# Optimization experiments

Hardware: AMD Instinct MI355X
Metric: run time of the kernel (lower is better)

## Reference

```python
import jax, jax.numpy as jnp
import numpy as np

EMBED_DIM = 1024
N_TOKENS = 4096


def setup_inputs() -> dict:
    key = jax.random.key(0)
    k1, k2, k3 = jax.random.split(key, 3)
    inputs = jax.random.normal(k1, (N_TOKENS, EMBED_DIM), dtype=jnp.float32)
    rotation_params = jax.random.normal(k2, (EMBED_DIM, EMBED_DIM), dtype=jnp.float32)
    entangle_params = jax.random.normal(k3, (EMBED_DIM, EMBED_DIM), dtype=jnp.float32)
    return {"inputs": inputs, "rotation_params": rotation_params, "entangle_params": entangle_params}


def reference(inputs, rotation_params, entangle_params):
    d = EMBED_DIM
    wq = rotation_params.reshape(d, -1)
    wk = entangle_params.reshape(d, -1)
    query = inputs @ wq                      # [N, d_k]
    key = inputs @ wk                        # [N, d_k]
    scale = 1.0 / np.sqrt(d).astype(np.float32)
    scores = jax.nn.softmax((query @ key.T) * scale, axis=-1)  # [N, N]
    return scores @ inputs                   # [N, d]
```

## Files before the change

kernel.cpp:

```cpp
#include <hip/hip_runtime.h>

#define EMBED 1024
#define NTOK  4096
#define MARGIN 256.0f
#define KC     8
#define CAP    128

#define SX_INV 25.4f
#define SQ_INV 0.0155029296875f
#define SCLOGIT 0.07936198f

typedef short  s16x8 __attribute__((ext_vector_type(8)));
typedef float  f32x4 __attribute__((ext_vector_type(4)));
typedef int    i32x4 __attribute__((ext_vector_type(4)));

__device__ __forceinline__ unsigned short f2bf(float f) {
    unsigned int u = __float_as_uint(f);
    u = (u + 0x7FFFu + ((u >> 16) & 1u)) >> 16;
    return (unsigned short)u;
}
__device__ __forceinline__ float bf2f(unsigned short h) {
    return __uint_as_float(((unsigned int)h) << 16);
}

__device__ __forceinline__ void async16(const void* g, void* l) {
    __builtin_amdgcn_global_load_lds(
        (const __attribute__((address_space(1))) unsigned int*)g,
        (__attribute__((address_space(3))) unsigned int*)l, 16, 0, 0);
}

template<int ROWS>
__device__ __forceinline__ void stage_rows(const char* __restrict__ g,
                                           int ld, char* lds, int wave, int lane) {
#pragma unroll
    for (int r = 0; r < ROWS / 64; ++r) {
        const int row0 = (wave * (ROWS / 64) + r) * 16;
        const int r_loc = lane >> 2;
        const int kc = (lane - (lane >> 3)) & 3;
        const char* gp = g + (size_t)(row0 + r_loc) * ld + kc * 16;
        char* lp = lds + row0 * 64;
        async16(gp, lp);
    }
}

__device__ __forceinline__ int frag_slot(int row, int kc) {
    return (kc + ((row & 15) >> 1)) & 3;
}
__device__ __forceinline__ s16x8 frag_bf16(const char* lds, int row, int kc) {
    return *(const s16x8*)(lds + row * 64 + frag_slot(row, kc) * 16);
}
__device__ __forceinline__ i32x4 frag_i8(const char* lds, int row, int kc) {
    return *(const i32x4*)(lds + row * 64 + frag_slot(row, kc) * 16);
}

template<int BM, int BN, int SPLIT, int EPI, int NCH>
__global__ __launch_bounds__(256) void gemm_mfma(
        const unsigned short* __restrict__ Ahi, const unsigned short* __restrict__ Alo,
        const unsigned short* __restrict__ Bhi, const unsigned short* __restrict__ Blo,
        float* __restrict__ C, unsigned short* __restrict__ Chi,
        unsigned short* __restrict__ Clo, signed char* __restrict__ Ci8,
        int K, int lda, int ldb, int ldc, float scale)
{
    constexpr int TM = BM / 2, TN = BN / 2;
    constexpr int IM = TM / 16, IN = TN / 16;

    __shared__ __align__(16) char As_hi[BM * 64 * NCH];
    __shared__ __align__(16) char Bs_hi[BN * 64 * NCH];
    __shared__ __align__(16) char As_lo[SPLIT == 3 ? BM * 64 * NCH : 16];
    __shared__ __align__(16) char Bs_lo[SPLIT == 3 ? BN * 64 * NCH : 16];

    const int t = threadIdx.x;
    const int lane = t & 63, wave = t >> 6;
    const int wm = wave >> 1, wn = wave & 1;
    const int m0 = blockIdx.y * BM, n0 = blockIdx.x * BN;

    f32x4 acc[IM][IN];
#pragma unroll
    for (int i = 0; i < IM; ++i)
#pragma unroll
        for (int j = 0; j < IN; ++j)
#pragma unroll
            for (int r = 0; r < 4; ++r) acc[i][j][r] = 0.f;

    const char* ah_g = (const char*)(Ahi + (size_t)m0 * lda);
    const char* bh_g = (const char*)(Bhi + (size_t)n0 * ldb);
    const char* al_g = (SPLIT == 3) ? (const char*)(Alo + (size_t)m0 * lda) : nullptr;
    const char* bl_g = (SPLIT == 3) ? (const char*)(Blo + (size_t)n0 * ldb) : nullptr;

    const int kc = lane >> 4;
    const int rr = lane & 15;

    for (int k0 = 0; k0 < K; k0 += 32 * NCH) {
#pragma unroll
        for (int c = 0; c < NCH; ++c) {
            const int kb = (k0 + 32 * c) * 2;
            stage_rows<BM>(ah_g + kb, lda * 2, As_hi + c * BM * 64, wave, lane);
            stage_rows<BN>(bh_g + kb, ldb * 2, Bs_hi + c * BN * 64, wave, lane);
            if constexpr (SPLIT == 3) {
                stage_rows<BM>(al_g + kb, lda * 2, As_lo + c * BM * 64, wave, lane);
                stage_rows<BN>(bl_g + kb, ldb * 2, Bs_lo + c * BN * 64, wave, lane);
            }
        }
        __syncthreads();

#pragma unroll
        for (int c = 0; c < NCH; ++c) {
            s16x8 ah[IM], bh[IN], al[IM], bl[IN];
#pragma unroll
            for (int i = 0; i < IM; ++i)
                ah[i] = frag_bf16(As_hi + c * BM * 64, wm * TM + i * 16 + rr, kc);
#pragma unroll
            for (int j = 0; j < IN; ++j)
                bh[j] = frag_bf16(Bs_hi + c * BN * 64, wn * TN + j * 16 + rr, kc);
            if constexpr (SPLIT == 3) {
#pragma unroll
                for (int i = 0; i < IM; ++i)
                    al[i] = frag_bf16(As_lo + c * BM * 64, wm * TM + i * 16 + rr, kc);
#pragma unroll
                for (int j = 0; j < IN; ++j)
                    bl[j] = frag_bf16(Bs_lo + c * BN * 64, wn * TN + j * 16 + rr, kc);
            }

#pragma unroll
            for (int i = 0; i < IM; ++i)
#pragma unroll
                for (int j = 0; j < IN; ++j)
                    acc[i][j] = __builtin_amdgcn_mfma_f32_16x16x32_bf16(ah[i], bh[j], acc[i][j], 0, 0, 0);
            if constexpr (SPLIT == 3) {
#pragma unroll
                for (int i = 0; i < IM; ++i)
#pragma unroll
                    for (int j = 0; j < IN; ++j)
                        acc[i][j] = __builtin_amdgcn_mfma_f32_16x16x32_bf16(ah[i], bl[j], acc[i][j], 0, 0, 0);
#pragma unroll
                for (int i = 0; i < IM; ++i)
#pragma unroll
                    for (int j = 0; j < IN; ++j)
                        acc[i][j] = __builtin_amdgcn_mfma_f32_16x16x32_bf16(al[i], bh[j], acc[i][j], 0, 0, 0);
            }
        }
        __syncthreads();
    }

    const int lr = lane >> 4;
    const int lc = lane & 15;
#pragma unroll
    for (int i = 0; i < IM; ++i)
#pragma unroll
        for (int j = 0; j < IN; ++j)
#pragma unroll
            for (int r = 0; r < 4; ++r) {
                const int row = m0 + wm * TM + i * 16 + lr * 4 + r;
                const int col = n0 + wn * TN + j * 16 + lc;
                const float v = acc[i][j][r] * scale;
                const size_t idx = (size_t)row * ldc + col;
                if constexpr (EPI == 1) {
                    const unsigned short h = f2bf(v);
                    Chi[idx] = h;
                    Clo[idx] = f2bf(v - bf2f(h));
                } else {
                    C[idx] = v;
                    const float q = fminf(fmaxf(v * SQ_INV, -127.f), 127.f);
                    Ci8[idx] = (signed char)(int)rintf(q);
                }
            }
}

__global__ __launch_bounds__(256) void gemm_i8_scores(
        const signed char* __restrict__ A,
        const signed char* __restrict__ B,
        float* __restrict__ tmax, int* __restrict__ cnts, int2* __restrict__ cand)
{
    __shared__ __align__(16) char As[128 * 64 * 2];
    __shared__ __align__(16) char Bs[128 * 64 * 2];

    const int t = threadIdx.x;
    const int lane = t & 63, wave = t >> 6;
    const int wm = wave >> 1, wn = wave & 1;
    const int m0 = blockIdx.y * 128, n0 = blockIdx.x * 128;

    i32x4 acc[4][4];
#pragma unroll
    for (int i = 0; i < 4; ++i)
#pragma unroll
        for (int j = 0; j < 4; ++j)
#pragma unroll
            for (int r = 0; r < 4; ++r) acc[i][j][r] = 0;

    const char* a_g = (const char*)A + (size_t)m0 * EMBED;
    const char* b_g = (const char*)B + (size_t)n0 * EMBED;
    const int kc = lane >> 4;
    const int rr = lane & 15;

    for (int k0 = 0; k0 < EMBED; k0 += 128) {
#pragma unroll
        for (int c = 0; c < 2; ++c) {
            stage_rows<128>(a_g + k0 + 64 * c, EMBED, As + c * 128 * 64, wave, lane);
            stage_rows<128>(b_g + k0 + 64 * c, EMBED, Bs + c * 128 * 64, wave, lane);
        }
        __syncthreads();

#pragma unroll
        for (int c = 0; c < 2; ++c) {
            i32x4 af[4], bf[4];
#pragma unroll
            for (int i = 0; i < 4; ++i) af[i] = frag_i8(As + c * 128 * 64, wm * 64 + i * 16 + rr, kc);
#pragma unroll
            for (int j = 0; j < 4; ++j) bf[j] = frag_i8(Bs + c * 128 * 64, wn * 64 + j * 16 + rr, kc);
#pragma unroll
            for (int i = 0; i < 4; ++i)
#pragma unroll
                for (int j = 0; j < 4; ++j)
                    acc[i][j] = __builtin_amdgcn_mfma_i32_16x16x64_i8(af[i], bf[j], acc[i][j], 0, 0, 0);
        }
        __syncthreads();
    }

    const int lr = lane >> 4;
    const int lc = lane & 15;
    const int wslot = blockIdx.x * 2 + wn;
    const unsigned long long grp = 0xFFFFull << (lr * 16);
    const unsigned long long low = (lane == 63) ? 0x7FFFFFFFFFFFFFFFull
                                                : ((1ull << lane) - 1);
#pragma unroll
    for (int i = 0; i < 4; ++i)
#pragma unroll
        for (int r = 0; r < 4; ++r) {
            const int row = m0 + wm * 64 + i * 16 + lr * 4 + r;
            float v[4];
            float vmax = -3.4e38f;
#pragma unroll
            for (int j = 0; j < 4; ++j) {
                v[j] = (float)acc[i][j][r] * SCLOGIT;
                vmax = fmaxf(vmax, v[j]);
            }
#pragma unroll
            for (int msk = 1; msk < 16; msk <<= 1)
                vmax = fmaxf(vmax, __shfl_xor(vmax, msk, 64));
            const float thr = vmax - MARGIN;
            int base = 0;
#pragma unroll
            for (int j = 0; j < 4; ++j) {
                const bool pred = v[j] > thr;
                const unsigned long long m = __ballot(pred) & grp;
                if (pred) {
                    const int pos = base + __popcll(m & low);
                    if (pos < KC)
                        cand[((size_t)row * 64 + wslot) * KC + pos] =
                            make_int2(n0 + wn * 64 + j * 16 + lc,
                                      __float_as_int(v[j]));
                }
                base += __popcll(m);
            }
            if (lc == 0) {
                tmax[(size_t)row * 64 + wslot] = vmax;
                cnts[(size_t)row * 64 + wslot] = base < KC ? base : KC;
            }
        }
}

__global__ __launch_bounds__(256) void split_all(
        const float4* __restrict__ X, const float4* __restrict__ Wq,
        const float4* __restrict__ Wk,
        ushort4* __restrict__ Xhi, ushort4* __restrict__ Xlo, char4* __restrict__ Xi8,
        ushort4* __restrict__ Wqhi, ushort4* __restrict__ Wqlo,
        ushort4* __restrict__ Wkhi, ushort4* __restrict__ Wklo) {
    const int NX4 = NTOK * EMBED / 4;
    const int NW4 = EMBED * EMBED / 4;
    const int n = blockIdx.x * 256 + threadIdx.x;

    const float4* src;
    ushort4 *hi, *lo;
    int idx;
    bool do_i8 = false;
    if (n < NX4) {
        src = X; hi = Xhi; lo = Xlo; idx = n; do_i8 = true;
    } else if (n < NX4 + NW4) {
        src = Wq; hi = Wqhi; lo = Wqlo; idx = n - NX4;
    } else {
        src = Wk; hi = Wkhi; lo = Wklo; idx = n - NX4 - NW4;
    }
    const float4 v = src[idx];
    ushort4 h, l;
    h.x = f2bf(v.x); l.x = f2bf(v.x - bf2f(h.x));
    h.y = f2bf(v.y); l.y = f2bf(v.y - bf2f(h.y));
    h.z = f2bf(v.z); l.z = f2bf(v.z - bf2f(h.z));
    h.w = f2bf(v.w); l.w = f2bf(v.w - bf2f(h.w));
    hi[idx] = h; lo[idx] = l;
    if (do_i8) {
        char4 c;
        c.x = (signed char)(int)rintf(fminf(fmaxf(v.x * SX_INV, -127.f), 127.f));
        c.y = (signed char)(int)rintf(fminf(fmaxf(v.y * SX_INV, -127.f), 127.f));
        c.z = (signed char)(int)rintf(fminf(fmaxf(v.z * SX_INV, -127.f), 127.f));
        c.w = (signed char)(int)rintf(fminf(fmaxf(v.w * SX_INV, -127.f), 127.f));
        Xi8[idx] = c;
    }
}

__global__ __launch_bounds__(256) void sparse_out(const float* __restrict__ tmax,
                                                  const int* __restrict__ cnts,
                                                  const int2* __restrict__ cand,
                                                  const float* __restrict__ Qf,
                                                  const float* __restrict__ X,
                                                  float* __restrict__ out) {
    const int t = threadIdx.x;
    const int lane = t & 63, wave = t >> 6;
    const int row = blockIdx.x;

    __shared__ float gmax_s;
    __shared__ int   n2;
    __shared__ int   list[CAP];
    __shared__ float ll[CAP];
    if (t == 0) n2 = 0;

    float gm = -3.4e38f;
    if (t < 64) gm = tmax[(size_t)row * 64 + t];
#pragma unroll
    for (int off = 32; off >= 1; off >>= 1) gm = fmaxf(gm, __shfl_xor(gm, off, 64));
    if (t == 0) gmax_s = gm;
    __syncthreads();
    const float thr = gmax_s - MARGIN;

    for (int e = t; e < 64 * KC; e += 256) {
        const int s = e >> 3, k = e & (KC - 1);
        if (k < cnts[(size_t)row * 64 + s]) {
            const int2 c = cand[((size_t)row * 64 + s) * KC + k];
            if (__int_as_float(c.y) > thr) {
                const int p = atomicAdd(&n2, 1);
                if (p < CAP) list[p] = c.x;
            }
        }
    }
    __syncthreads();
    const int nc = min(n2, CAP);

    float4 q[4];
#pragma unroll
    for (int i = 0; i < 4; ++i)
        q[i] = *(const float4*)&Qf[(size_t)row * EMBED + lane * 16 + i * 4];
    for (int c = wave; c < nc; c += 4) {
        const float* xp = &X[(size_t)list[c] * EMBED + lane * 16];
        float p = 0.f;
#pragma unroll
        for (int i = 0; i < 4; ++i) {
            const float4 x4 = *(const float4*)(xp + i * 4);
            p += q[i].x * x4.x + q[i].y * x4.y + q[i].z * x4.z + q[i].w * x4.w;
        }
#pragma unroll
        for (int off = 32; off >= 1; off >>= 1) p += __shfl_xor(p, off, 64);
        if (lane == 0) ll[c] = p * 0.03125f;
    }
    __syncthreads();

    float mt = -3.4e38f;
    for (int c = 0; c < nc; ++c) mt = fmaxf(mt, ll[c]);
    float wsum = 0.f;
    for (int c = 0; c < nc; ++c) wsum += __expf(ll[c] - mt);
    const float inv = 1.0f / wsum;

    float4 o = {0.f, 0.f, 0.f, 0.f};
    for (int c = 0; c < nc; ++c) {
        const float w = __expf(ll[c] - mt);
        const float4 xj = *(const float4*)&X[(size_t)list[c] * EMBED + t * 4];
        o.x += w * xj.x; o.y += w * xj.y; o.z += w * xj.z; o.w += w * xj.w;
    }
    o.x *= inv; o.y *= inv; o.z *= inv; o.w *= inv;
    *(float4*)&out[(size_t)row * EMBED + t * 4] = o;
}

extern "C" void kernel_launch(void* const* d_in, const int* in_sizes, int n_in,
                              void* d_out, int out_size, void* d_ws, size_t ws_size,
                              hipStream_t stream) {
    const float* X  = (const float*)d_in[0];
    const float* Wq = (const float*)d_in[1];
    const float* Wk = (const float*)d_in[2];
    float* out = (float*)d_out;

    char* ws = (char*)d_ws;
    const size_t MB = 1024 * 1024;
    unsigned short* Xhi = (unsigned short*)(ws + 0 * MB);
    unsigned short* Xlo = (unsigned short*)(ws + 8 * MB);
    signed char*    Xi8 = (signed char*)(ws + 16 * MB);
    float*          Qf  = (float*)(ws + 20 * MB);
    signed char*    Qi8 = (signed char*)(ws + 36 * MB);
    float* tmax = (float*)(ws + 40 * MB);
    int*   cnts = (int*)(ws + 41 * MB);
    int2*  cand = (int2*)(ws + 42 * MB);
    unsigned short* Wqhi = (unsigned short*)(ws + 58 * MB);
    unsigned short* Wqlo = (unsigned short*)(ws + 60 * MB);
    unsigned short* Wkhi = (unsigned short*)(ws + 62 * MB);
    unsigned short* Wklo = (unsigned short*)(ws + 64 * MB);
    unsigned short* Thi  = (unsigned short*)(ws + 66 * MB);
    unsigned short* Tlo  = (unsigned short*)(ws + 68 * MB);

    split_all<<<6144, 256, 0, stream>>>(
        (const float4*)X, (const float4*)Wq, (const float4*)Wk,
        (ushort4*)Xhi, (ushort4*)Xlo, (char4*)Xi8,
        (ushort4*)Wqhi, (ushort4*)Wqlo, (ushort4*)Wkhi, (ushort4*)Wklo);

    gemm_mfma<64, 64, 3, 1, 2><<<dim3(16, 16), 256, 0, stream>>>(
        Wkhi, Wklo, Wqhi, Wqlo, nullptr, Thi, Tlo, nullptr,
        EMBED, EMBED, EMBED, EMBED, 1.0f);

    gemm_mfma<128, 64, 3, 2, 2><<<dim3(16, 32), 256, 0, stream>>>(
        Xhi, Xlo, Thi, Tlo, Qf, nullptr, nullptr, Qi8,
        EMBED, EMBED, EMBED, EMBED, 1.0f);

    gemm_i8_scores<<<dim3(32, 32), 256, 0, stream>>>(Qi8, Xi8, tmax, cnts, cand);

    sparse_out<<<NTOK, 256, 0, stream>>>(tmax, cnts, cand, Qf, X, out);
}
```

Before: 183.7 us.

## Split-K the weight-product GEMM and overlap X conversion in the same launch

The 1024x1024 T = Wk*Wq^T product (Wk, Wq being the rotation and entangle weights) now uses a 4-way split-K over 1024 blocks instead of 256, raising occupancy. Its K loop stages hi and lo tiles and issues three bf16 MFMAs per step. The same grid carries extra z-slices that convert X to bf16 hi/lo and int8, so that conversion runs alongside the GEMM. A new merge kernel sums the four fp32 partials and splits them into hi/lo, which adds a launch and 16MB of partial traffic. The partials buffer reuses workspace later used by cand, which is safe because the merge runs before the scores kernel writes cand.

```diff
diff --git a/kernel.cpp b/kernel.cpp
--- a/kernel.cpp
+++ b/kernel.cpp
@@ -166,6 +166,162 @@
             }
 }
 
+__global__ __launch_bounds__(256) void t_fused(
+        const unsigned short* __restrict__ Ahi, const unsigned short* __restrict__ Alo,
+        const unsigned short* __restrict__ Bhi, const unsigned short* __restrict__ Blo,
+        float* __restrict__ Cpart,
+        const float4* __restrict__ X, ushort4* __restrict__ Xhi,
+        ushort4* __restrict__ Xlo, char4* __restrict__ Xi8)
+{
+    constexpr int BM = 64, BN = 64, NCH = 2;
+    __shared__ __align__(16) char As_hi[BM * 64 * NCH];
+    __shared__ __align__(16) char Bs_hi[BN * 64 * NCH];
+    __shared__ __align__(16) char As_lo[BM * 64 * NCH];
+    __shared__ __align__(16) char Bs_lo[BN * 64 * NCH];
+
+    const int t = threadIdx.x;
+    const int z = blockIdx.z;
+
+    if (z >= 4) {
+        const int idx = (((z - 4) * 256) + blockIdx.y * 16 + blockIdx.x) * 256 + t;
+        const float4 v = X[idx];
+        ushort4 h, l;
+        h.x = f2bf(v.x); l.x = f2bf(v.x - bf2f(h.x));
+        h.y = f2bf(v.y); l.y = f2bf(v.y - bf2f(h.y));
+        h.z = f2bf(v.z); l.z = f2bf(v.z - bf2f(h.z));
+        h.w = f2bf(v.w); l.w = f2bf(v.w - bf2f(h.w));
+        Xhi[idx] = h; Xlo[idx] = l;
+        char4 c;
+        c.x = (signed char)(int)rintf(fminf(fmaxf(v.x * SX_INV, -127.f), 127.f));
+        c.y = (signed char)(int)rintf(fminf(fmaxf(v.y * SX_INV, -127.f), 127.f));
+        c.z = (signed char)(int)rintf(fminf(fmaxf(v.z * SX_INV, -127.f), 127.f));
+        c.w = (signed char)(int)rintf(fminf(fmaxf(v.w * SX_INV, -127.f), 127.f));
+        Xi8[idx] = c;
+        return;
+    }
+
+    const int lane = t & 63, wave = t >> 6;
+    const int wm = wave >> 1, wn = wave & 1;
+    const int m0 = blockIdx.y * BM, n0 = blockIdx.x * BN;
+
+    f32x4 acc[2][2];
+#pragma unroll
+    for (int i = 0; i < 2; ++i)
+#pragma unroll
+        for (int j = 0; j < 2; ++j)
+#pragma unroll
+            for (int r = 0; r < 4; ++r) acc[i][j][r] = 0.f;
+
+    const char* ah_g = (const char*)(Ahi + (size_t)m0 * EMBED);
+    const char* bh_g = (const char*)(Bhi + (size_t)n0 * EMBED);
+    const char* al_g = (const char*)(Alo + (size_t)m0 * EMBED);
+    const char* bl_g = (const char*)(Blo + (size_t)n0 * EMBED);
+
+    const int kc = lane >> 4;
+    const int rr = lane & 15;
+    const int kbeg = z * 256;
+
+    for (int k0 = kbeg; k0 < kbeg + 256; k0 += 32 * NCH) {
+#pragma unroll
+        for (int c = 0; c < NCH; ++c) {
+            const int kb = (k0 + 32 * c) * 2;
+            stage_rows<BM>(ah_g + kb, EMBED * 2, As_hi + c * BM * 64, wave, lane);
+            stage_rows<BN>(bh_g + kb, EMBED * 2, Bs_hi + c * BN * 64, wave, lane);
+            stage_rows<BM>(al_g + kb, EMBED * 2, As_lo + c * BM * 64, wave, lane);
+            stage_rows<BN>(bl_g + kb, EMBED * 2, Bs_lo + c * BN * 64, wave, lane);
+        }
+        __syncthreads();
+
+#pragma unroll
+        for (int c = 0; c < NCH; ++c) {
+            s16x8 ah[2], bh[2], al[2], bl[2];
+#pragma unroll
+            for (int i = 0; i < 2; ++i)
+                ah[i] = frag_bf16(As_hi + c * BM * 64, wm * 32 + i * 16 + rr, kc);
+#pragma unroll
+            for (int j = 0; j < 2; ++j)
+                bh[j] = frag_bf16(Bs_hi + c * BN * 64, wn * 32 + j * 16 + rr, kc);
+#pragma unroll
+            for (int i = 0; i < 2; ++i)
+                al[i] = frag_bf16(As_lo + c * BM * 64, wm * 32 + i * 16 + rr, kc);
+#pragma unroll
+            for (int j = 0; j < 2; ++j)
+                bl[j] = frag_bf16(Bs_lo + c * BN * 64, wn * 32 + j * 16 + rr, kc);
+
+#pragma unroll
+            for (int i = 0; i < 2; ++i)
+#pragma unroll
+                for (int j = 0; j < 2; ++j)
+                    acc[i][j] = __builtin_amdgcn_mfma_f32_16x16x32_bf16(ah[i], bh[j], acc[i][j], 0, 0, 0);
+#pragma unroll
+            for (int i = 0; i < 2; ++i)
+#pragma unroll
+                for (int j = 0; j < 2; ++j)
+                    acc[i][j] = __builtin_amdgcn_mfma_f32_16x16x32_bf16(ah[i], bl[j], acc[i][j], 0, 0, 0);
+#pragma unroll
+            for (int i = 0; i < 2; ++i)
+#pragma unroll
+                for (int j = 0; j < 2; ++j)
+                    acc[i][j] = __builtin_amdgcn_mfma_f32_16x16x32_bf16(al[i], bh[j], acc[i][j], 0, 0, 0);
+        }
+        __syncthreads();
+    }
+
+    const int lr = lane >> 4;
+    const int lc = lane & 15;
+    float* Cz = Cpart + (size_t)z * EMBED * EMBED;
+#pragma unroll
+    for (int i = 0; i < 2; ++i)
+#pragma unroll
+        for (int j = 0; j < 2; ++j)
+#pragma unroll
+            for (int r = 0; r < 4; ++r) {
+                const int row = m0 + wm * 32 + i * 16 + lr * 4 + r;
+                const int col = n0 + wn * 32 + j * 16 + lc;
+                Cz[(size_t)row * EMBED + col] = acc[i][j][r];
+            }
+}
+
+__global__ __launch_bounds__(256) void t_merge(const float4* __restrict__ P,
+                                               ushort4* __restrict__ Thi,
+                                               ushort4* __restrict__ Tlo) {
+    const int idx = blockIdx.x * 256 + threadIdx.x;
+    const int S = EMBED * EMBED / 4;
+    const float4 a = P[idx], b = P[idx + S], c = P[idx + 2 * S], d = P[idx + 3 * S];
+    float4 s;
+    s.x = (a.x + b.x) + (c.x + d.x);
+    s.y = (a.y + b.y) + (c.y + d.y);
+    s.z = (a.z + b.z) + (c.z + d.z);
+    s.w = (a.w + b.w) + (c.w + d.w);
+    ushort4 h, l;
+    h.x = f2bf(s.x); l.x = f2bf(s.x - bf2f(h.x));
+    h.y = f2bf(s.y); l.y = f2bf(s.y - bf2f(h.y));
+    h.z = f2bf(s.z); l.z = f2bf(s.z - bf2f(h.z));
+    h.w = f2bf(s.w); l.w = f2bf(s.w - bf2f(h.w));
+    Thi[idx] = h; Tlo[idx] = l;
+}
+
+__global__ __launch_bounds__(256) void split_w(
+        const float4* __restrict__ Wq, const float4* __restrict__ Wk,
+        ushort4* __restrict__ Wqhi, ushort4* __restrict__ Wqlo,
+        ushort4* __restrict__ Wkhi, ushort4* __restrict__ Wklo) {
+    const int NW4 = EMBED * EMBED / 4;
+    const int n = blockIdx.x * 256 + threadIdx.x;
+
+    const float4* src;
+    ushort4 *hi, *lo;
+    int idx;
+    if (n < NW4) { src = Wq; hi = Wqhi; lo = Wqlo; idx = n; }
+    else         { src = Wk; hi = Wkhi; lo = Wklo; idx = n - NW4; }
+    const float4 v = src[idx];
+    ushort4 h, l;
+    h.x = f2bf(v.x); l.x = f2bf(v.x - bf2f(h.x));
+    h.y = f2bf(v.y); l.y = f2bf(v.y - bf2f(h.y));
+    h.z = f2bf(v.z); l.z = f2bf(v.z - bf2f(h.z));
+    h.w = f2bf(v.w); l.w = f2bf(v.w - bf2f(h.w));
+    hi[idx] = h; lo[idx] = l;
+}
+
 __global__ __launch_bounds__(256) void gemm_i8_scores(
         const signed char* __restrict__ A,
         const signed char* __restrict__ B,
@@ -257,44 +413,6 @@
                 cnts[(size_t)row * 64 + wslot] = base < KC ? base : KC;
             }
         }
-}
-
-__global__ __launch_bounds__(256) void split_all(
-        const float4* __restrict__ X, const float4* __restrict__ Wq,
-        const float4* __restrict__ Wk,
-        ushort4* __restrict__ Xhi, ushort4* __restrict__ Xlo, char4* __restrict__ Xi8,
-        ushort4* __restrict__ Wqhi, ushort4* __restrict__ Wqlo,
-        ushort4* __restrict__ Wkhi, ushort4* __restrict__ Wklo) {
-    const int NX4 = NTOK * EMBED / 4;
-    const int NW4 = EMBED * EMBED / 4;
-    const int n = blockIdx.x * 256 + threadIdx.x;
-
-    const float4* src;
-    ushort4 *hi, *lo;
-    int idx;
-    bool do_i8 = false;
-    if (n < NX4) {
-        src = X; hi = Xhi; lo = Xlo; idx = n; do_i8 = true;
-    } else if (n < NX4 + NW4) {
-        src = Wq; hi = Wqhi; lo = Wqlo; idx = n - NX4;
-    } else {
-        src = Wk; hi = Wkhi; lo = Wklo; idx = n - NX4 - NW4;
-    }
-    const float4 v = src[idx];
-    ushort4 h, l;
-    h.x = f2bf(v.x); l.x = f2bf(v.x - bf2f(h.x));
-    h.y = f2bf(v.y); l.y = f2bf(v.y - bf2f(h.y));
-    h.z = f2bf(v.z); l.z = f2bf(v.z - bf2f(h.z));
-    h.w = f2bf(v.w); l.w = f2bf(v.w - bf2f(h.w));
-    hi[idx] = h; lo[idx] = l;
-    if (do_i8) {
-        char4 c;
-        c.x = (signed char)(int)rintf(fminf(fmaxf(v.x * SX_INV, -127.f), 127.f));
-        c.y = (signed char)(int)rintf(fminf(fmaxf(v.y * SX_INV, -127.f), 127.f));
-        c.z = (signed char)(int)rintf(fminf(fmaxf(v.z * SX_INV, -127.f), 127.f));
-        c.w = (signed char)(int)rintf(fminf(fmaxf(v.w * SX_INV, -127.f), 127.f));
-        Xi8[idx] = c;
-    }
 }
 
 __global__ __launch_bounds__(256) void sparse_out(const float* __restrict__ tmax,
@@ -392,15 +510,18 @@
     unsigned short* Wklo = (unsigned short*)(ws + 64 * MB);
     unsigned short* Thi  = (unsigned short*)(ws + 66 * MB);
     unsigned short* Tlo  = (unsigned short*)(ws + 68 * MB);
-
-    split_all<<<6144, 256, 0, stream>>>(
-        (const float4*)X, (const float4*)Wq, (const float4*)Wk,
-        (ushort4*)Xhi, (ushort4*)Xlo, (char4*)Xi8,
+    float* Tpart = (float*)(ws + 42 * MB);
+
+    split_w<<<2048, 256, 0, stream>>>(
+        (const float4*)Wq, (const float4*)Wk,
         (ushort4*)Wqhi, (ushort4*)Wqlo, (ushort4*)Wkhi, (ushort4*)Wklo);
 
-    gemm_mfma<64, 64, 3, 1, 2><<<dim3(16, 16), 256, 0, stream>>>(
-        Wkhi, Wklo, Wqhi, Wqlo, nullptr, Thi, Tlo, nullptr,
-        EMBED, EMBED, EMBED, EMBED, 1.0f);
+    t_fused<<<dim3(16, 16, 20), 256, 0, stream>>>(
+        Wkhi, Wklo, Wqhi, Wqlo, Tpart,
+        (const float4*)X, (ushort4*)Xhi, (ushort4*)Xlo, (char4*)Xi8);
+
+    t_merge<<<1024, 256, 0, stream>>>((const float4*)Tpart,
+                                      (ushort4*)Thi, (ushort4*)Tlo);
 
     gemm_mfma<128, 64, 3, 2, 2><<<dim3(16, 32), 256, 0, stream>>>(
         Xhi, Xlo, Thi, Tlo, Qf, nullptr, nullptr, Qi8,
```

Measured after the change: 183.2 us. About the same (-0.2%).
